# Kernel tuning notes

Hardware: AMD Instinct MI355X
Metric: run time of the kernel (lower is better)

## Reference

```python
import jax, jax.numpy as jnp
import numpy as np

N_NODES = 200000
N_EDGES = 3200000


def _gcn_prep(edge_index, n_nodes):
    # Add self loops (PyG GCNConv default) and compute symmetric normalization.
    loops = jnp.arange(n_nodes, dtype=edge_index.dtype)
    src = jnp.concatenate([edge_index[0], loops])
    dst = jnp.concatenate([edge_index[1], loops])
    deg = jax.ops.segment_sum(jnp.ones_like(dst, dtype=jnp.float32), dst,
                              num_segments=n_nodes)
    dinv = jnp.where(deg > 0, jax.lax.rsqrt(deg), 0.0)
    norm = dinv[src] * dinv[dst]  # [E+N]
    return src, dst, norm


def _gcn_conv(x, src, dst, norm, W, b, n_nodes):
    h = x @ W                                   # [N, out]
    msg = h[src] * norm[:, None]                # gather + scale, [E+N, out]
    out = jax.ops.segment_sum(msg, dst, num_segments=n_nodes)  # scatter-add
    return out + b


def setup_inputs() -> dict:
    key = jax.random.key(0)
    k = jax.random.split(key, 4)
    x = jax.random.normal(k[0], (N_NODES, 4), dtype=jnp.float32)
    edge_index = jax.random.randint(k[1], (2, N_EDGES), 0, N_NODES, dtype=jnp.int64)
    W1 = jax.random.normal(k[2], (4, 16), dtype=jnp.float32) * (1.0 / np.sqrt(4))
    b1 = jnp.zeros((16,), dtype=jnp.float32)
    W2 = jax.random.normal(k[3], (16, 1), dtype=jnp.float32) * (1.0 / np.sqrt(16))
    b2 = jnp.zeros((1,), dtype=jnp.float32)
    return {"x": x, "edge_index": edge_index, "W1": W1, "b1": b1,
            "W2": W2, "b2": b2}


def reference(x, edge_index, W1, b1, W2, b2):
    n = x.shape[0]
    src, dst, norm = _gcn_prep(edge_index, n)
    h = _gcn_conv(x, src, dst, norm, W1, b1, n)
    h = jax.nn.relu(h)
    out = _gcn_conv(h, src, dst, norm, W2, b2, n)
    return out
```

## Files before the change

kernel.cpp:

```cpp
#include <hip/hip_runtime.h>


#define BSE   512
#define CH    16384
#define NBW   512
#define SH    9
#define NB    391
#define FCAP  10752
#define BSB   512
#define RSTG  ((FCAP + BSB - 1) / BSB)
#define NOEDGE 0xFFFFFFFFu

__global__ void k_bin(const int* __restrict__ src, const int* __restrict__ dst,
                      int E, unsigned* __restrict__ gcur,
                      unsigned* __restrict__ epack) {
    __shared__ unsigned cnt[NB];
    __shared__ unsigned cur[NB];
    __shared__ unsigned basec[NB];
    int b = blockIdx.x, t = threadIdx.x;
    for (int i = t; i < NB; i += BSE) cnt[i] = 0;
    __syncthreads();
    int lo = b * CH, hi = min(E, lo + CH);
    int aligned = (hi - lo) & ~3;
    for (int i = lo + 4 * t; i + 3 < hi; i += 4 * BSE) {
        int4 d4 = *(const int4*)(dst + i);
        atomicAdd(&cnt[((unsigned)d4.x) >> SH], 1u);
        atomicAdd(&cnt[((unsigned)d4.y) >> SH], 1u);
        atomicAdd(&cnt[((unsigned)d4.z) >> SH], 1u);
        atomicAdd(&cnt[((unsigned)d4.w) >> SH], 1u);
    }
    for (int i = lo + aligned + t; i < hi; i += BSE)
        atomicAdd(&cnt[((unsigned)dst[i]) >> SH], 1u);
    __syncthreads();
    for (int i = t; i < NB; i += BSE) {
        unsigned c = cnt[i];
        unsigned pad = (c + 15u) & ~15u;
        unsigned ofs = pad ? atomicAdd(&gcur[i], pad) : 0u;
        unsigned base = (unsigned)i * FCAP + ofs;
        basec[i] = base;
        cur[i] = base;
    }
    __syncthreads();
    for (int i = lo + 4 * t; i + 3 < hi; i += 4 * BSE) {
        int4 d4 = *(const int4*)(dst + i);
        int4 s4 = *(const int4*)(src + i);
        unsigned k0 = ((unsigned)d4.x) >> SH, k1 = ((unsigned)d4.y) >> SH;
        unsigned k2 = ((unsigned)d4.z) >> SH, k3 = ((unsigned)d4.w) >> SH;
        unsigned p0 = atomicAdd(&cur[k0], 1u);
        unsigned p1 = atomicAdd(&cur[k1], 1u);
        unsigned p2 = atomicAdd(&cur[k2], 1u);
        unsigned p3 = atomicAdd(&cur[k3], 1u);
        if (p0 < (k0 + 1u) * FCAP) epack[p0] = ((unsigned)s4.x << SH) | (((unsigned)d4.x) & (NBW - 1u));
        if (p1 < (k1 + 1u) * FCAP) epack[p1] = ((unsigned)s4.y << SH) | (((unsigned)d4.y) & (NBW - 1u));
        if (p2 < (k2 + 1u) * FCAP) epack[p2] = ((unsigned)s4.z << SH) | (((unsigned)d4.z) & (NBW - 1u));
        if (p3 < (k3 + 1u) * FCAP) epack[p3] = ((unsigned)s4.w << SH) | (((unsigned)d4.w) & (NBW - 1u));
    }
    for (int i = lo + aligned + t; i < hi; i += BSE) {
        unsigned d = (unsigned)dst[i];
        unsigned k = d >> SH;
        unsigned pos = atomicAdd(&cur[k], 1u);
        if (pos < (k + 1u) * FCAP)
            epack[pos] = ((unsigned)src[i] << SH) | (d & (NBW - 1u));
    }
    __syncthreads();
    for (int i = t; i < NB; i += BSE) {
        unsigned end = basec[i] + ((cnt[i] + 15u) & ~15u);
        unsigned kend = ((unsigned)i + 1u) * FCAP;
        if (end > kend) end = kend;
        for (unsigned p = cur[i]; p < end; ++p) epack[p] = NOEDGE;
    }
}

__global__ void k_build(unsigned* __restrict__ epack, const unsigned* __restrict__ gcur,
                        const float* __restrict__ x,
                        unsigned* __restrict__ meta,
                        float* __restrict__ x_scaled, int N) {
    __shared__ unsigned stage[FCAP];
    __shared__ unsigned cnt[BSB];
    __shared__ unsigned cur[BSB];
    __shared__ unsigned wsum[BSB / 64];
    __shared__ unsigned s_lenv;
    const int k = blockIdx.x, t = threadIdx.x;
    const unsigned base = (unsigned)k * FCAP;
    const int len = min((int)gcur[k], FCAP);
    unsigned r[RSTG];
    #pragma unroll
    for (int j = 0; j < RSTG; ++j) {
        int i = t + j * BSB;
        r[j] = (i < len) ? epack[base + i] : NOEDGE;
    }
    cnt[t] = 0;
    __syncthreads();
    #pragma unroll
    for (int j = 0; j < RSTG; ++j) {
        unsigned p = r[j];
        if (p != NOEDGE) atomicAdd(&cnt[p & (NBW - 1u)], 1u);
    }
    __syncthreads();
    const unsigned c = cnt[t];
    unsigned v = c;
    #pragma unroll
    for (int off = 1; off < 64; off <<= 1) {
        unsigned u = __shfl_up(v, off);
        if ((t & 63) >= off) v += u;
    }
    if ((t & 63) == 63) wsum[t >> 6] = v;
    __syncthreads();
    if (t < BSB / 64) {
        unsigned w = wsum[t];
        #pragma unroll
        for (int off = 1; off < BSB / 64; off <<= 1) {
            unsigned u = __shfl_up(w, off);
            if (t >= off) w += u;
        }
        wsum[t] = w;
    }
    __syncthreads();
    const unsigned incl = v + ((t >> 6) ? wsum[(t >> 6) - 1] : 0u);
    const unsigned excl = incl - c;
    cur[t] = excl;
    if (t == BSB - 1) s_lenv = incl;
    const int node = k * NBW + t;
    if (node < N) {
        meta[node] = excl | (c << 14);
        float di = rsqrtf((float)(c + 1u));
        float4 xv = ((const float4*)x)[node];
        ((float4*)x_scaled)[node] = make_float4(xv.x * di, xv.y * di, xv.z * di, xv.w * di);
    }
    __syncthreads();
    #pragma unroll
    for (int j = 0; j < RSTG; ++j) {
        unsigned p = r[j];
        if (p != NOEDGE) {
            unsigned pos = atomicAdd(&cur[p & (NBW - 1u)], 1u);
            stage[pos] = p >> SH;
        }
    }
    __syncthreads();
    const int lenv = (int)s_lenv;
    for (int i = 4 * t; i + 3 < lenv; i += 4 * BSB)
        *(int4*)(epack + base + i) = *(const int4*)&stage[i];
    if (t < (lenv & 3)) epack[base + (lenv & ~3) + t] = stage[(lenv & ~3) + t];
}

__global__ void k_agg1(const unsigned* __restrict__ esorted, const unsigned* __restrict__ meta,
                       const float* __restrict__ x_scaled,
                       const float* __restrict__ W1, const float* __restrict__ b1,
                       const float* __restrict__ W2,
                       float* __restrict__ z_scaled, int N) {
    int node = blockIdx.x * blockDim.x + threadIdx.x;
    if (node >= N) return;
    unsigned m = meta[node];
    unsigned c = m >> 14;
    unsigned lo = (unsigned)(node >> SH) * FCAP + (m & 16383u);
    unsigned hi = lo + c;
    float di = rsqrtf((float)(c + 1u));
    const float4* xs4 = (const float4*)x_scaled;
    float4 a0 = xs4[node];
    float4 a1 = make_float4(0.f, 0.f, 0.f, 0.f);
    float4 a2 = make_float4(0.f, 0.f, 0.f, 0.f);
    float4 a3 = make_float4(0.f, 0.f, 0.f, 0.f);
    unsigned i = lo;
    for (; i + 3 < hi; i += 4) {
        float4 v0 = xs4[esorted[i]],     v1 = xs4[esorted[i + 1]];
        float4 v2 = xs4[esorted[i + 2]], v3 = xs4[esorted[i + 3]];
        a0.x += v0.x; a0.y += v0.y; a0.z += v0.z; a0.w += v0.w;
        a1.x += v1.x; a1.y += v1.y; a1.z += v1.z; a1.w += v1.w;
        a2.x += v2.x; a2.y += v2.y; a2.z += v2.z; a2.w += v2.w;
        a3.x += v3.x; a3.y += v3.y; a3.z += v3.z; a3.w += v3.w;
    }
    for (; i < hi; ++i) {
        float4 v = xs4[esorted[i]];
        a0.x += v.x; a0.y += v.y; a0.z += v.z; a0.w += v.w;
    }
    float p0 = di * (a0.x + a1.x + a2.x + a3.x);
    float p1 = di * (a0.y + a1.y + a2.y + a3.y);
    float p2 = di * (a0.z + a1.z + a2.z + a3.z);
    float p3 = di * (a0.w + a1.w + a2.w + a3.w);
    float z = 0.0f;
    #pragma unroll
    for (int cc = 0; cc < 16; ++cc) {
        float h1 = p0 * W1[0 * 16 + cc] + p1 * W1[1 * 16 + cc]
                 + p2 * W1[2 * 16 + cc] + p3 * W1[3 * 16 + cc] + b1[cc];
        h1 = fmaxf(h1, 0.0f);
        z += h1 * W2[cc];
    }
    z_scaled[node] = z * di;
}

__global__ void k_agg2(const unsigned* __restrict__ esorted, const unsigned* __restrict__ meta,
                       const float* __restrict__ z_scaled,
                       const float* __restrict__ b2, float* __restrict__ out, int N) {
    int node = blockIdx.x * blockDim.x + threadIdx.x;
    if (node >= N) return;
    unsigned m = meta[node];
    unsigned c = m >> 14;
    unsigned lo = (unsigned)(node >> SH) * FCAP + (m & 16383u);
    unsigned hi = lo + c;
    float di = rsqrtf((float)(c + 1u));
    float a0 = z_scaled[node], a1 = 0.f, a2 = 0.f, a3 = 0.f;
    unsigned i = lo;
    for (; i + 3 < hi; i += 4) {
        a0 += z_scaled[esorted[i]];
        a1 += z_scaled[esorted[i + 1]];
        a2 += z_scaled[esorted[i + 2]];
        a3 += z_scaled[esorted[i + 3]];
    }
    for (; i < hi; ++i) a0 += z_scaled[esorted[i]];
    out[node] = di * (a0 + a1 + a2 + a3) + b2[0];
}

extern "C" void kernel_launch(void* const* d_in, const int* in_sizes, int n_in,
                              void* d_out, int out_size, void* d_ws, size_t ws_size,
                              hipStream_t stream) {
    const float* x  = (const float*)d_in[0];
    const int*   ei = (const int*)d_in[1];
    const float* W1 = (const float*)d_in[2];
    const float* b1 = (const float*)d_in[3];
    const float* W2 = (const float*)d_in[4];
    const float* b2 = (const float*)d_in[5];

    const int N = in_sizes[0] / 4;
    const int E = in_sizes[1] / 2;
    const int* src = ei;
    const int* dst = ei + E;
    const int NA = (E + CH - 1) / CH;

    char* ws = (char*)d_ws;
    unsigned* gcur     = (unsigned*)ws;  ws += 4096;
    unsigned* epack    = (unsigned*)ws;  ws += (size_t)NB * FCAP * 4;
    unsigned* meta     = (unsigned*)ws;  ws += (size_t)N * 4;
    float*    x_scaled = (float*)ws;     ws += (size_t)N * 4 * 4;
    float*    z_scaled = (float*)ws;     ws += (size_t)N * 4;
    float* out = (float*)d_out;

    hipMemsetAsync(gcur, 0, NB * sizeof(unsigned), stream);
    k_bin  <<<NA, BSE, 0, stream>>>(src, dst, E, gcur, epack);
    k_build<<<NB, BSB, 0, stream>>>(epack, gcur, x, meta, x_scaled, N);
    k_agg1 <<<(N + 255) / 256, 256, 0, stream>>>(epack, meta, x_scaled,
                                                 W1, b1, W2, z_scaled, N);
    k_agg2 <<<(N + 255) / 256, 256, 0, stream>>>(epack, meta, z_scaled, b2, out, N);
}
```

Before: 169.9 us.

## Stage binned edges in LDS and write them out contiguously per bucket

The binning kernel now computes a block-wide prefix sum of the per-bucket counts and scatters packed edges into a shared-memory staging buffer, ordered by bucket. A second pass then copies the staged entries to global memory in linear order, locating each entry's bucket by binary search over the offsets. This replaces scattered per-element global writes with mostly contiguous runs per bucket, aiming to improve write coalescing. In exchange it uses 64KB of LDS per block, which lowers occupancy, and adds scan and search overhead.

```diff
diff --git a/kernel.cpp b/kernel.cpp
--- a/kernel.cpp
+++ b/kernel.cpp
@@ -14,60 +14,101 @@
 __global__ void k_bin(const int* __restrict__ src, const int* __restrict__ dst,
                       int E, unsigned* __restrict__ gcur,
                       unsigned* __restrict__ epack) {
+    __shared__ unsigned stage[CH];
     __shared__ unsigned cnt[NB];
-    __shared__ unsigned cur[NB];
-    __shared__ unsigned basec[NB];
-    int b = blockIdx.x, t = threadIdx.x;
+    __shared__ unsigned ofs[NB + 1];
+    __shared__ unsigned curp[NB];
+    __shared__ unsigned gbase[NB];
+    __shared__ unsigned wsum[BSE / 64];
+    const int b = blockIdx.x, t = threadIdx.x;
     for (int i = t; i < NB; i += BSE) cnt[i] = 0;
     __syncthreads();
-    int lo = b * CH, hi = min(E, lo + CH);
-    int aligned = (hi - lo) & ~3;
-    for (int i = lo + 4 * t; i + 3 < hi; i += 4 * BSE) {
-        int4 d4 = *(const int4*)(dst + i);
+    const int lo = b * CH, hi = min(E, lo + CH);
+    const int n = hi - lo;
+    const int aligned = n & ~3;
+    for (int i = 4 * t; i + 3 < n; i += 4 * BSE) {
+        int4 d4 = *(const int4*)(dst + lo + i);
         atomicAdd(&cnt[((unsigned)d4.x) >> SH], 1u);
         atomicAdd(&cnt[((unsigned)d4.y) >> SH], 1u);
         atomicAdd(&cnt[((unsigned)d4.z) >> SH], 1u);
         atomicAdd(&cnt[((unsigned)d4.w) >> SH], 1u);
     }
-    for (int i = lo + aligned + t; i < hi; i += BSE)
-        atomicAdd(&cnt[((unsigned)dst[i]) >> SH], 1u);
-    __syncthreads();
-    for (int i = t; i < NB; i += BSE) {
-        unsigned c = cnt[i];
+    for (int i = aligned + t; i < n; i += BSE)
+        atomicAdd(&cnt[((unsigned)dst[lo + i]) >> SH], 1u);
+    __syncthreads();
+    const unsigned c = (t < NB) ? cnt[t] : 0u;
+    unsigned v = c;
+    #pragma unroll
+    for (int off = 1; off < 64; off <<= 1) {
+        unsigned u = __shfl_up(v, off);
+        if ((t & 63) >= off) v += u;
+    }
+    if ((t & 63) == 63) wsum[t >> 6] = v;
+    __syncthreads();
+    if (t < BSE / 64) {
+        unsigned w = wsum[t];
+        #pragma unroll
+        for (int off = 1; off < BSE / 64; off <<= 1) {
+            unsigned u = __shfl_up(w, off);
+            if (t >= off) w += u;
+        }
+        wsum[t] = w;
+    }
+    __syncthreads();
+    const unsigned incl = v + ((t >> 6) ? wsum[(t >> 6) - 1] : 0u);
+    const unsigned excl = incl - c;
+    if (t < NB) {
+        ofs[t] = excl;
+        curp[t] = excl;
         unsigned pad = (c + 15u) & ~15u;
-        unsigned ofs = pad ? atomicAdd(&gcur[i], pad) : 0u;
-        unsigned base = (unsigned)i * FCAP + ofs;
-        basec[i] = base;
-        cur[i] = base;
-    }
-    __syncthreads();
-    for (int i = lo + 4 * t; i + 3 < hi; i += 4 * BSE) {
-        int4 d4 = *(const int4*)(dst + i);
-        int4 s4 = *(const int4*)(src + i);
+        unsigned o = pad ? atomicAdd(&gcur[t], pad) : 0u;
+        gbase[t] = (unsigned)t * FCAP + o;
+    }
+    if (t == NB - 1) ofs[NB] = incl;
+    __syncthreads();
+    for (int i = 4 * t; i + 3 < n; i += 4 * BSE) {
+        int4 d4 = *(const int4*)(dst + lo + i);
+        int4 s4 = *(const int4*)(src + lo + i);
         unsigned k0 = ((unsigned)d4.x) >> SH, k1 = ((unsigned)d4.y) >> SH;
         unsigned k2 = ((unsigned)d4.z) >> SH, k3 = ((unsigned)d4.w) >> SH;
-        unsigned p0 = atomicAdd(&cur[k0], 1u);
-        unsigned p1 = atomicAdd(&cur[k1], 1u);
-        unsigned p2 = atomicAdd(&cur[k2], 1u);
-        unsigned p3 = atomicAdd(&cur[k3], 1u);
-        if (p0 < (k0 + 1u) * FCAP) epack[p0] = ((unsigned)s4.x << SH) | (((unsigned)d4.x) & (NBW - 1u));
-        if (p1 < (k1 + 1u) * FCAP) epack[p1] = ((unsigned)s4.y << SH) | (((unsigned)d4.y) & (NBW - 1u));
-        if (p2 < (k2 + 1u) * FCAP) epack[p2] = ((unsigned)s4.z << SH) | (((unsigned)d4.z) & (NBW - 1u));
-        if (p3 < (k3 + 1u) * FCAP) epack[p3] = ((unsigned)s4.w << SH) | (((unsigned)d4.w) & (NBW - 1u));
-    }
-    for (int i = lo + aligned + t; i < hi; i += BSE) {
-        unsigned d = (unsigned)dst[i];
+        unsigned p0 = atomicAdd(&curp[k0], 1u);
+        unsigned p1 = atomicAdd(&curp[k1], 1u);
+        unsigned p2 = atomicAdd(&curp[k2], 1u);
+        unsigned p3 = atomicAdd(&curp[k3], 1u);
+        stage[p0] = ((unsigned)s4.x << SH) | (((unsigned)d4.x) & (NBW - 1u));
+        stage[p1] = ((unsigned)s4.y << SH) | (((unsigned)d4.y) & (NBW - 1u));
+        stage[p2] = ((unsigned)s4.z << SH) | (((unsigned)d4.z) & (NBW - 1u));
+        stage[p3] = ((unsigned)s4.w << SH) | (((unsigned)d4.w) & (NBW - 1u));
+    }
+    for (int i = aligned + t; i < n; i += BSE) {
+        unsigned d = (unsigned)dst[lo + i];
         unsigned k = d >> SH;
-        unsigned pos = atomicAdd(&cur[k], 1u);
-        if (pos < (k + 1u) * FCAP)
-            epack[pos] = ((unsigned)src[i] << SH) | (d & (NBW - 1u));
-    }
-    __syncthreads();
+        unsigned pos = atomicAdd(&curp[k], 1u);
+        stage[pos] = ((unsigned)src[lo + i] << SH) | (d & (NBW - 1u));
+    }
+    __syncthreads();
+    for (int p0 = 4 * t; p0 < n; p0 += 4 * BSE) {
+        unsigned k = 0;
+        #pragma unroll
+        for (unsigned s = 256; s; s >>= 1) {
+            unsigned cand = k + s;
+            if (cand <= NB && ofs[cand] <= (unsigned)p0) k = cand;
+        }
+        #pragma unroll
+        for (int j = 0; j < 4; ++j) {
+            int p = p0 + j;
+            if (p >= n) break;
+            while (ofs[k + 1] <= (unsigned)p) ++k;
+            unsigned addr = gbase[k] + ((unsigned)p - ofs[k]);
+            if (addr < (k + 1u) * FCAP) epack[addr] = stage[p];
+        }
+    }
     for (int i = t; i < NB; i += BSE) {
-        unsigned end = basec[i] + ((cnt[i] + 15u) & ~15u);
+        unsigned s = gbase[i] + cnt[i];
+        unsigned e = gbase[i] + ((cnt[i] + 15u) & ~15u);
         unsigned kend = ((unsigned)i + 1u) * FCAP;
-        if (end > kend) end = kend;
-        for (unsigned p = cur[i]; p < end; ++p) epack[p] = NOEDGE;
+        if (e > kend) e = kend;
+        for (unsigned p = s; p < e; ++p) epack[p] = NOEDGE;
     }
 }
 
```

After: 163.1 us (median of 2 runs). -4.0%, faster.
